# Performance work log

Hardware: AMD Instinct MI355X
Metric: run time of the kernel (lower is better)

Reference implementation:

```python
import jax, jax.numpy as jnp
import numpy as np

N = 16384      # number of points (pixels)
C = 64         # value channels of U
D_REF = 5      # bilateral reference feature dim (xy + rgb)


def setup_inputs() -> dict:
    key = jax.random.key(0)
    k1, k2 = jax.random.split(key)
    U = jax.random.normal(k1, (N, C), dtype=jnp.float32)
    ref = jax.random.normal(k2, (N, D_REF), dtype=jnp.float32)
    return {"U": U, "ref": ref}


def reference(U, ref):
    # Gaussian filtering on reference features (exact form of the LSH-approx filter):
    #   out[i] = sum_j exp(-0.5 * ||ref_i - ref_j||^2) * U[j]  -  U[i]
    sq = jnp.sum(ref * ref, axis=-1)                      # [N]
    d2 = sq[:, None] + sq[None, :] - 2.0 * (ref @ ref.T)  # [N, N] squared distances
    K = jnp.exp(-0.5 * jnp.maximum(d2, 0.0))              # [N, N] Gaussian kernel
    return K @ U - U                                       # [N, C]
```

## Files before the change

kernel.cpp:

```cpp
#include <hip/hip_runtime.h>
#include <hip/hip_bf16.h>
#include <stdint.h>

#define N_PTS 16384
#define C_CH  64
#define D_REF 5
#define LOG2E 1.44269504088896340736f
#define IBLOCKS 64

typedef __attribute__((ext_vector_type(8))) short bf16x8;
typedef __attribute__((ext_vector_type(4))) float f32x4;

__device__ __forceinline__ unsigned short bf16rn(float v) {
    unsigned u = __builtin_bit_cast(unsigned, v) + 0x8000u;
    return (unsigned short)(u >> 16);
}
__device__ __forceinline__ float bf16tof(unsigned short h) {
    unsigned u = ((unsigned)h) << 16;
    return __builtin_bit_cast(float, u);
}
__device__ __forceinline__ unsigned pack2bf16(float lo, float hi) {
    unsigned a = __builtin_bit_cast(unsigned, lo) + 0x8000u;
    unsigned b = __builtin_bit_cast(unsigned, hi) + 0x8000u;
    return __builtin_amdgcn_perm(b, a, 0x07060302u);
}
__device__ __forceinline__ float fast_exp2(float x) {
#if __has_builtin(__builtin_amdgcn_exp2f)
    return __builtin_amdgcn_exp2f(x);
#else
    return exp2f(x);
#endif
}

__device__ __forceinline__ void dma16(const unsigned short* g, unsigned short* l) {
#if __has_builtin(__builtin_amdgcn_global_load_lds)
    __builtin_amdgcn_global_load_lds(
        (const __attribute__((address_space(1))) unsigned int*)g,
        (__attribute__((address_space(3))) unsigned int*)l, 16, 0, 0);
#else
    const int lane = threadIdx.x & 63;
    *(uint4*)(l + lane * 8) = *(const uint4*)(g);
#endif
}

__global__ __launch_bounds__(256) void prep_all(
    const float* __restrict__ U, const float* __restrict__ ref,
    unsigned short* __restrict__ packA, unsigned short* __restrict__ packB,
    unsigned short* __restrict__ utPack)
{
    __shared__ unsigned short tile[64 * 80];
    const int bid = blockIdx.x;
    const int t   = threadIdx.x;

    if (bid < 512) {
        const int gid  = bid * 256 + t;
        const int half = gid >> 16;
        const int id   = gid & 0xFFFF;
        const int tile16 = id >> 6;
        const int lane = id & 63;
        const int q    = lane >> 4;
        const int m    = lane & 15;
        const int p = half ? (tile16 * 16 + m)
                           : ((tile16 >> 1) * 32 + (m >> 2) * 8 + (m & 3) + (tile16 & 1) * 4);

        const float* r = ref + (size_t)p * D_REF;
        float rv[5];
        float sq = 0.f;
#pragma unroll
        for (int d = 0; d < 5; ++d) { rv[d] = r[d]; sq += rv[d] * rv[d]; }
        const float h = -0.5f * LOG2E * sq;

        unsigned short bh[5], bl[5];
#pragma unroll
        for (int d = 0; d < 5; ++d) {
            const float base = half ? rv[d] * LOG2E : rv[d];
            bh[d] = bf16rn(base);
            bl[d] = bf16rn(base - bf16tof(bh[d]));
        }
        const unsigned short hh  = bf16rn(h);
        const unsigned short hl  = bf16rn(h - bf16tof(hh));
        const unsigned short one = 0x3F80;

        unsigned short outv[8];
#pragma unroll
        for (int tt = 0; tt < 8; ++tt) {
            const int k = q * 8 + tt;
            unsigned short v = 0;
            if (!half) {
                if      (k < 5)   v = bh[k];
                else if (k < 10)  v = bh[k - 5];
                else if (k < 15)  v = bl[k - 10];
                else if (k == 15) v = hh;
                else if (k == 16) v = hl;
                else if (k <= 18) v = one;
            } else {
                if      (k < 5)   v = bh[k];
                else if (k < 10)  v = bl[k - 5];
                else if (k < 15)  v = bh[k - 10];
                else if (k <= 16) v = one;
                else if (k == 17) v = hh;
                else if (k == 18) v = hl;
            }
            outv[tt] = v;
        }
        unsigned short* dst = (half ? packB : packA) + ((size_t)tile16 * 64 + lane) * 8;
        *(uint4*)dst = *(uint4*)outv;
    } else {
        const int b  = bid - 512;
        const int j0 = b * 64;
        const int c  = t & 63;
        const int jb = t >> 6;
#pragma unroll
        for (int k = 0; k < 16; ++k) {
            const int jr = jb + k * 4;
            tile[c * 80 + jr] = bf16rn(U[(size_t)(j0 + jr) * C_CH + c]);
        }
        __syncthreads();
#pragma unroll
        for (int rep = 0; rep < 2; ++rep) {
            const int id   = rep * 256 + t;
            const int lane = id & 63;
            const int ct   = (id >> 6) & 3;
            const int kt   = id >> 8;
            const int m    = lane & 15;
            const int q    = lane >> 4;
            const int cc   = ct * 16 + m;
            const int jloc = kt * 32 + q * 8;
            const uint4 frag = *(const uint4*)&tile[cc * 80 + jloc];
            const int jtile  = b * 2 + kt;
            *(uint4*)&utPack[(((size_t)jtile * 4 + ct) * 64 + lane) * 8] = frag;
        }
    }
}

template<int JS>
__global__ __launch_bounds__(256, 4) void lsh_main(
    const float* __restrict__ U,
    const unsigned short* __restrict__ packA,
    const unsigned short* __restrict__ packB,
    const unsigned short* __restrict__ utPack,
    float* __restrict__ part,
    float* __restrict__ out,
    int use_part)
{
    constexpr int CHUNKS = (N_PTS / JS) / 128;
    __shared__ __align__(16) unsigned short sh[12288];

    const int t    = threadIdx.x;
    const int lane = t & 63;
    const int wave = t >> 6;
    const int q    = lane >> 4;
    const int m    = lane & 15;

    const int ib = blockIdx.x / JS;
    const int js = blockIdx.x % JS;

    bf16x8 bfrag[4];
#pragma unroll
    for (int s = 0; s < 4; ++s) {
        const int itile = ib * 16 + wave * 4 + s;
        bfrag[s] = *(const bf16x8*)(packB + ((size_t)itile * 64 + lane) * 8);
    }

    f32x4 acc[4][4];
#pragma unroll
    for (int s = 0; s < 4; ++s)
#pragma unroll
        for (int ct = 0; ct < 4; ++ct) acc[s][ct] = (f32x4){0.f, 0.f, 0.f, 0.f};

    for (int chunk = 0; chunk < CHUNKS; ++chunk) {
        const unsigned short* srcU = utPack + (size_t)(js * CHUNKS + chunk) * 8192;
        const unsigned short* srcA = packA  + (size_t)(js * CHUNKS + chunk) * 4096;
        __syncthreads();
#pragma unroll
        for (int r = 0; r < 4; ++r)
            dma16(srcU + r * 2048 + wave * 512 + lane * 8, sh + r * 2048 + wave * 512);
#pragma unroll
        for (int r = 0; r < 2; ++r)
            dma16(srcA + r * 2048 + wave * 512 + lane * 8, sh + 8192 + r * 2048 + wave * 512);
        __syncthreads();

#pragma unroll
        for (int kt = 0; kt < 4; ++kt) {
            const bf16x8 ga0 = *(const bf16x8*)(sh + 8192 + (kt * 2 + 0) * 512 + lane * 8);
            const bf16x8 ga1 = *(const bf16x8*)(sh + 8192 + (kt * 2 + 1) * 512 + lane * 8);

            const f32x4 z = (f32x4){0.f, 0.f, 0.f, 0.f};
            bf16x8 sfrag[4];
#pragma unroll
            for (int s = 0; s < 4; ++s) {
                const f32x4 g0 = __builtin_amdgcn_mfma_f32_16x16x32_bf16(ga0, bfrag[s], z, 0, 0, 0);
                const f32x4 g1 = __builtin_amdgcn_mfma_f32_16x16x32_bf16(ga1, bfrag[s], z, 0, 0, 0);
                union { unsigned u[4]; bf16x8 v; } sb;
                sb.u[0] = pack2bf16(fast_exp2(g0[0]), fast_exp2(g0[1]));
                sb.u[1] = pack2bf16(fast_exp2(g0[2]), fast_exp2(g0[3]));
                sb.u[2] = pack2bf16(fast_exp2(g1[0]), fast_exp2(g1[1]));
                sb.u[3] = pack2bf16(fast_exp2(g1[2]), fast_exp2(g1[3]));
                sfrag[s] = sb.v;
            }
#pragma unroll
            for (int ct = 0; ct < 4; ++ct) {
                const bf16x8 uf = *(const bf16x8*)(sh + kt * 2048 + ct * 512 + lane * 8);
#pragma unroll
                for (int s = 0; s < 4; ++s)
                    acc[s][ct] = __builtin_amdgcn_mfma_f32_16x16x32_bf16(
                        uf, sfrag[s], acc[s][ct], 0, 0, 0);
            }
        }
    }

    if (use_part) {
        float* dst = part + ((size_t)js * IBLOCKS + ib) * (256 * C_CH);
#pragma unroll
        for (int s = 0; s < 4; ++s) {
            const int i_loc = (wave * 4 + s) * 16 + m;
#pragma unroll
            for (int ct = 0; ct < 4; ++ct)
                *(f32x4*)(dst + i_loc * C_CH + ct * 16 + q * 4) = acc[s][ct];
        }
    } else {
#pragma unroll
        for (int s = 0; s < 4; ++s) {
            const int i_glob = ib * 256 + (wave * 4 + s) * 16 + m;
#pragma unroll
            for (int ct = 0; ct < 4; ++ct)
#pragma unroll
                for (int r2 = 0; r2 < 4; ++r2) {
                    const int c = ct * 16 + q * 4 + r2;
                    float val = acc[s][ct][r2];
                    if (js == 0) val -= U[(size_t)i_glob * C_CH + c];
                    atomicAdd(&out[(size_t)i_glob * C_CH + c], val);
                }
        }
    }
}

template<int JS>
__global__ __launch_bounds__(256) void reduce_part(
    const f32x4* __restrict__ part, const f32x4* __restrict__ U,
    f32x4* __restrict__ out)
{
    const int x = blockIdx.x * 256 + threadIdx.x;
    f32x4 s = part[x];
#pragma unroll
    for (int js = 1; js < JS; ++js)
        s += part[((size_t)js << 18) + x];
    out[x] = s - U[x];
}

extern "C" void kernel_launch(void* const* d_in, const int* in_sizes, int n_in,
                              void* d_out, int out_size, void* d_ws, size_t ws_size,
                              hipStream_t stream) {
    const float* U   = (const float*)d_in[0];
    const float* ref = (const float*)d_in[1];
    float* out = (float*)d_out;

    unsigned short* utPack = (unsigned short*)d_ws;
    unsigned short* packA  = (unsigned short*)((char*)d_ws + (size_t)2 * 1024 * 1024);
    unsigned short* packB  = (unsigned short*)((char*)d_ws + (size_t)3 * 1024 * 1024);
    float*          part   = (float*)((char*)d_ws + (size_t)4 * 1024 * 1024);

    const size_t MB = 1024 * 1024;
    prep_all<<<768, 256, 0, stream>>>(U, ref, packA, packB, utPack);

    if (ws_size >= (4 + 4 * 16) * MB) {
        lsh_main<16><<<IBLOCKS * 16, 256, 0, stream>>>(U, packA, packB, utPack,
                                                       part, out, 1);
        reduce_part<16><<<1024, 256, 0, stream>>>((const f32x4*)part,
                                                  (const f32x4*)U, (f32x4*)out);
    } else if (ws_size >= (4 + 4 * 8) * MB) {
        lsh_main<8><<<IBLOCKS * 8, 256, 0, stream>>>(U, packA, packB, utPack,
                                                     part, out, 1);
        reduce_part<8><<<1024, 256, 0, stream>>>((const f32x4*)part,
                                                 (const f32x4*)U, (f32x4*)out);
    } else {
        hipMemsetAsync(d_out, 0, (size_t)out_size * sizeof(float), stream);
        lsh_main<8><<<IBLOCKS * 8, 256, 0, stream>>>(U, packA, packB, utPack,
                                                     part, out, 0);
    }
}
```

Before: 126.5 us.

## Load packed fragments directly from global memory, dropping LDS staging and barriers

The main loop no longer stages U and A tiles into shared memory with async global-to-LDS copies and two __syncthreads per chunk. Each wave now reads its bf16 fragments straight from global memory (L2-resident) per 32-column unit, and prefetches the next A fragments one iteration ahead. The MFMA/exp2 ordering is also interleaved in pairs to expose more independent work. This removes barrier and LDS traffic, but every wave in a block now fetches the same data separately, and global-load latency for the U fragments is not hidden by a prefetch.

After: 130.2 us. +3.0%, slower.

```diff
diff --git a/kernel.cpp b/kernel.cpp
--- a/kernel.cpp
+++ b/kernel.cpp
@@ -29,17 +29,6 @@
     return __builtin_amdgcn_exp2f(x);
 #else
     return exp2f(x);
-#endif
-}
-
-__device__ __forceinline__ void dma16(const unsigned short* g, unsigned short* l) {
-#if __has_builtin(__builtin_amdgcn_global_load_lds)
-    __builtin_amdgcn_global_load_lds(
-        (const __attribute__((address_space(1))) unsigned int*)g,
-        (__attribute__((address_space(3))) unsigned int*)l, 16, 0, 0);
-#else
-    const int lane = threadIdx.x & 63;
-    *(uint4*)(l + lane * 8) = *(const uint4*)(g);
 #endif
 }
 
@@ -143,8 +132,7 @@
     float* __restrict__ out,
     int use_part)
 {
-    constexpr int CHUNKS = (N_PTS / JS) / 128;
-    __shared__ __align__(16) unsigned short sh[12288];
+    constexpr int UNITS = (N_PTS / JS) / 32;
 
     const int t    = threadIdx.x;
     const int lane = t & 63;
@@ -168,45 +156,52 @@
 #pragma unroll
         for (int ct = 0; ct < 4; ++ct) acc[s][ct] = (f32x4){0.f, 0.f, 0.f, 0.f};
 
-    for (int chunk = 0; chunk < CHUNKS; ++chunk) {
-        const unsigned short* srcU = utPack + (size_t)(js * CHUNKS + chunk) * 8192;
-        const unsigned short* srcA = packA  + (size_t)(js * CHUNKS + chunk) * 4096;
-        __syncthreads();
-#pragma unroll
-        for (int r = 0; r < 4; ++r)
-            dma16(srcU + r * 2048 + wave * 512 + lane * 8, sh + r * 2048 + wave * 512);
-#pragma unroll
-        for (int r = 0; r < 2; ++r)
-            dma16(srcA + r * 2048 + wave * 512 + lane * 8, sh + 8192 + r * 2048 + wave * 512);
-        __syncthreads();
-
-#pragma unroll
-        for (int kt = 0; kt < 4; ++kt) {
-            const bf16x8 ga0 = *(const bf16x8*)(sh + 8192 + (kt * 2 + 0) * 512 + lane * 8);
-            const bf16x8 ga1 = *(const bf16x8*)(sh + 8192 + (kt * 2 + 1) * 512 + lane * 8);
-
-            const f32x4 z = (f32x4){0.f, 0.f, 0.f, 0.f};
-            bf16x8 sfrag[4];
-#pragma unroll
-            for (int s = 0; s < 4; ++s) {
-                const f32x4 g0 = __builtin_amdgcn_mfma_f32_16x16x32_bf16(ga0, bfrag[s], z, 0, 0, 0);
-                const f32x4 g1 = __builtin_amdgcn_mfma_f32_16x16x32_bf16(ga1, bfrag[s], z, 0, 0, 0);
-                union { unsigned u[4]; bf16x8 v; } sb;
-                sb.u[0] = pack2bf16(fast_exp2(g0[0]), fast_exp2(g0[1]));
-                sb.u[1] = pack2bf16(fast_exp2(g0[2]), fast_exp2(g0[3]));
-                sb.u[2] = pack2bf16(fast_exp2(g1[0]), fast_exp2(g1[1]));
-                sb.u[3] = pack2bf16(fast_exp2(g1[2]), fast_exp2(g1[3]));
-                sfrag[s] = sb.v;
-            }
-#pragma unroll
-            for (int ct = 0; ct < 4; ++ct) {
-                const bf16x8 uf = *(const bf16x8*)(sh + kt * 2048 + ct * 512 + lane * 8);
-#pragma unroll
-                for (int s = 0; s < 4; ++s)
-                    acc[s][ct] = __builtin_amdgcn_mfma_f32_16x16x32_bf16(
-                        uf, sfrag[s], acc[s][ct], 0, 0, 0);
-            }
-        }
+    const unsigned short* pA = packA  + ((size_t)js * UNITS) * 1024 + lane * 8;
+    const unsigned short* pU = utPack + ((size_t)js * UNITS) * 2048 + lane * 8;
+
+    bf16x8 ga0 = *(const bf16x8*)pA;
+    bf16x8 ga1 = *(const bf16x8*)(pA + 512);
+
+    for (int u = 0; u < UNITS; ++u) {
+        bf16x8 nga0 = ga0, nga1 = ga1;
+        if (u + 1 < UNITS) {
+            nga0 = *(const bf16x8*)(pA + 1024);
+            nga1 = *(const bf16x8*)(pA + 1536);
+        }
+
+        const f32x4 z = (f32x4){0.f, 0.f, 0.f, 0.f};
+        bf16x8 sfrag[4];
+#pragma unroll
+        for (int sp = 0; sp < 2; ++sp) {
+            f32x4 g0a = __builtin_amdgcn_mfma_f32_16x16x32_bf16(ga0, bfrag[sp*2+0], z, 0, 0, 0);
+            f32x4 g1a = __builtin_amdgcn_mfma_f32_16x16x32_bf16(ga1, bfrag[sp*2+0], z, 0, 0, 0);
+            f32x4 g0b = __builtin_amdgcn_mfma_f32_16x16x32_bf16(ga0, bfrag[sp*2+1], z, 0, 0, 0);
+            f32x4 g1b = __builtin_amdgcn_mfma_f32_16x16x32_bf16(ga1, bfrag[sp*2+1], z, 0, 0, 0);
+            union { unsigned u[4]; bf16x8 v; } sa, sb;
+            sa.u[0] = pack2bf16(fast_exp2(g0a[0]), fast_exp2(g0a[1]));
+            sa.u[1] = pack2bf16(fast_exp2(g0a[2]), fast_exp2(g0a[3]));
+            sa.u[2] = pack2bf16(fast_exp2(g1a[0]), fast_exp2(g1a[1]));
+            sa.u[3] = pack2bf16(fast_exp2(g1a[2]), fast_exp2(g1a[3]));
+            sb.u[0] = pack2bf16(fast_exp2(g0b[0]), fast_exp2(g0b[1]));
+            sb.u[1] = pack2bf16(fast_exp2(g0b[2]), fast_exp2(g0b[3]));
+            sb.u[2] = pack2bf16(fast_exp2(g1b[0]), fast_exp2(g1b[1]));
+            sb.u[3] = pack2bf16(fast_exp2(g1b[2]), fast_exp2(g1b[3]));
+            sfrag[sp*2+0] = sa.v;
+            sfrag[sp*2+1] = sb.v;
+        }
+#pragma unroll
+        for (int ct = 0; ct < 4; ++ct) {
+            const bf16x8 uf = *(const bf16x8*)(pU + ct * 512);
+#pragma unroll
+            for (int s = 0; s < 4; ++s)
+                acc[s][ct] = __builtin_amdgcn_mfma_f32_16x16x32_bf16(
+                    uf, sfrag[s], acc[s][ct], 0, 0, 0);
+        }
+
+        pA += 1024;
+        pU += 2048;
+        ga0 = nga0;
+        ga1 = nga1;
     }
 
     if (use_part) {
```
